# Kernel tuning notes

Hardware: AMD Instinct MI355X
Metric: run time of the kernel (lower is better)

## Reference

```python
import jax, jax.numpy as jnp
import numpy as np

S, H, T = 65536, 768, 6   # seq_len, hidden, n_types
K, WIN = 3, 15            # top-k starts, end-pointer window
TYPE_THRESH, START_THRESH = 0.3, 0.15


def setup_inputs() -> dict:
    key = jax.random.key(0)
    ks = jax.random.split(key, 9)
    sc = 0.02
    return {
        "token_embeds": jax.random.normal(ks[0], (S, H), dtype=jnp.float32),
        "W_start": jax.random.normal(ks[1], (H, T), dtype=jnp.float32) * sc,
        "b_start": jnp.zeros((T,), dtype=jnp.float32),
        "W_end": jax.random.normal(ks[2], (H, T), dtype=jnp.float32) * sc,
        "b_end": jnp.zeros((T,), dtype=jnp.float32),
        "W1": jax.random.normal(ks[3], (H, 64), dtype=jnp.float32) * sc,
        "b1": jnp.zeros((64,), dtype=jnp.float32),
        "W2": jax.random.normal(ks[4], (64, T), dtype=jnp.float32) * sc,
        "b2": jnp.zeros((T,), dtype=jnp.float32),
    }


def reference(token_embeds, W_start, b_start, W_end, b_end, W1, b1, W2, b2):
    # Pointer projections: (S, T)
    start_scores = token_embeds @ W_start + b_start
    end_scores = token_embeds @ W_end + b_end

    # Type confidence head on mean-pooled embedding (torch nn.GELU = exact erf)
    pooled = token_embeds.mean(axis=0)                      # (H,)
    h = jax.nn.gelu(pooled @ W1 + b1, approximate=False)    # (64,)
    type_conf = jax.nn.sigmoid(h @ W2 + b2)                 # (T,)

    # Softmax over sequence dim per type, then top-3 candidate starts per type
    s_probs = jax.nn.softmax(start_scores, axis=0)          # (S, T)
    top_vals, top_idx = jax.lax.top_k(s_probs.T, K)         # (T, K)

    # Windowed argmax over end_scores[s : s+15, t]
    pos = top_idx[:, :, None] + jnp.arange(WIN)
    in_range = pos < S
    pos_c = jnp.clip(pos, 0, S - 1)
    end_T = end_scores.T                                    # (T, S)
    window_vals = end_T[jnp.arange(T)[:, None, None], pos_c]
    window_vals = jnp.where(in_range, window_vals, -jnp.inf)
    e_off = jnp.argmax(window_vals, axis=-1)                # (T, K)

    starts = top_idx                                        # (T, K) int
    ends = top_idx + e_off + 1                              # exclusive end, matches e+1
    valid = (type_conf[:, None] >= TYPE_THRESH) & (top_vals >= START_THRESH)
    conf = jnp.where(valid, top_vals * type_conf[:, None], 0.0)  # (T, K)

    return conf, starts, ends, valid
```

## Files before the change

kernel.cpp:

```cpp
#include <hip/hip_runtime.h>
#include <math.h>

#define S_TOK 65536
#define H_DIM 768
#define T_TYPES 6
#define K_TOP 3
#define WIN 15
#define NBLK1 512
#define NWAVES (NBLK1 * 4)
#define ROWS_PER_WAVE (S_TOK / NWAVES)
#define POOL_CHUNKS 8
#define BLK_PER_CHUNK (NBLK1 / POOL_CHUNKS)

__device__ __forceinline__ void top3_insert(float v, int i,
    float& v0, float& v1, float& v2, int& i0, int& i1, int& i2)
{
    if (v > v0 || (v == v0 && i < i0)) {
        v2 = v1; i2 = i1; v1 = v0; i1 = i0; v0 = v; i0 = i;
    } else if (v > v1 || (v == v1 && i < i1)) {
        v2 = v1; i2 = i1; v1 = v; i1 = i;
    } else if (v > v2 || (v == v2 && i < i2)) {
        v2 = v; i2 = i;
    }
}

__device__ __forceinline__ void merge_state(
    float& M, float& se, float& v0, float& v1, float& v2,
    int& i0, int& i1, int& i2,
    float Mb, float seb, float w0, float w1, float w2,
    int j0, int j1, int j2)
{
    const float Mn = fmaxf(M, Mb);
    se = se * expf(M - Mn) + seb * expf(Mb - Mn);
    M = Mn;
    top3_insert(w0, j0, v0, v1, v2, i0, i1, i2);
    top3_insert(w1, j1, v0, v1, v2, i0, i1, i2);
    top3_insert(w2, j2, v0, v1, v2, i0, i1, i2);
}

__global__ __launch_bounds__(256, 2) void k_scores(
    const float* __restrict__ emb,
    const float* __restrict__ Wstart, const float* __restrict__ bstart,
    const float* __restrict__ Wend,   const float* __restrict__ bend,
    float* __restrict__ endS,
    float* __restrict__ partials,
    float* __restrict__ pooledPart)
{
    const int lane = threadIdx.x & 63;
    const int wib  = threadIdx.x >> 6;
    const int wave = blockIdx.x * 4 + wib;

    float wS[3][4][T_TYPES], wE[3][4][T_TYPES];
#pragma unroll
    for (int j = 0; j < 3; ++j)
#pragma unroll
        for (int c = 0; c < 4; ++c) {
            const int h = 4 * (lane + 64 * j) + c;
#pragma unroll
            for (int t = 0; t < T_TYPES; ++t) {
                wS[j][c][t] = Wstart[h * T_TYPES + t];
                wE[j][c][t] = Wend  [h * T_TYPES + t];
            }
        }

    float myBias = 0.0f;
    if (lane < T_TYPES)            myBias = bstart[lane];
    else if (lane < 2 * T_TYPES)   myBias = bend[lane - T_TYPES];

    float pool[3][4] = {};

    float M  = -3.402823466e38f, se = 0.0f;
    float v0 = -3.402823466e38f, v1 = v0, v2 = v0;
    int   i0 = -1, i1 = -1, i2 = -1;

    const int r0 = wave * ROWS_PER_WAVE;
    const float4* rowp = (const float4*)emb + (size_t)r0 * (H_DIM / 4);
    float4 c0 = rowp[lane], c1 = rowp[lane + 64], c2 = rowp[lane + 128];

    for (int r = r0; r < r0 + ROWS_PER_WAVE; ++r) {
        const float4* nextp = rowp + ((r + 1 < S_TOK) ? (H_DIM / 4) : 0);
        float4 n0 = nextp[lane], n1 = nextp[lane + 64], n2 = nextp[lane + 128];

        float acc[12];
#pragma unroll
        for (int a = 0; a < 12; ++a) acc[a] = 0.0f;

        const float4 ee[3] = {c0, c1, c2};
#pragma unroll
        for (int j = 0; j < 3; ++j) {
            const float ev[4] = {ee[j].x, ee[j].y, ee[j].z, ee[j].w};
#pragma unroll
            for (int c = 0; c < 4; ++c) {
                const float v = ev[c];
                pool[j][c] += v;
#pragma unroll
                for (int t = 0; t < T_TYPES; ++t) {
                    acc[t]           = fmaf(v, wS[j][c][t], acc[t]);
                    acc[T_TYPES + t] = fmaf(v, wE[j][c][t], acc[T_TYPES + t]);
                }
            }
        }

#pragma unroll
        for (int a = 0; a < 12; ++a) {
#pragma unroll
            for (int m = 1; m < 64; m <<= 1)
                acc[a] += __shfl_xor(acc[a], m, 64);
        }

        float v = acc[0];
#pragma unroll
        for (int a = 1; a < 12; ++a) v = (lane == a) ? acc[a] : v;
        v += myBias;

        if (lane < T_TYPES) {
            if (v > M) {
                se = se * expf(M - v) + 1.0f;
                v2 = v1; i2 = i1; v1 = v0; i1 = i0; v0 = v; i0 = r;
                M = v;
            } else {
                se += expf(v - M);
                if (v > v2 || (v == v2 && r < i2)) {
                    if (v > v1 || (v == v1 && r < i1)) {
                        v2 = v1; i2 = i1; v1 = v; i1 = r;
                    } else { v2 = v; i2 = r; }
                }
            }
        } else if (lane < 2 * T_TYPES) {
            endS[(size_t)(lane - T_TYPES) * S_TOK + r] = v;
        }

        c0 = n0; c1 = n1; c2 = n2; rowp = nextp;
    }

    if (lane < T_TYPES) {
        float* p = partials + ((size_t)wave * T_TYPES + lane) * 8;
        p[0] = M;  p[1] = se; p[2] = v0; p[3] = v1; p[4] = v2;
        p[5] = __int_as_float(i0);
        p[6] = __int_as_float(i1);
        p[7] = __int_as_float(i2);
    }

    __shared__ float lds[4][H_DIM];
#pragma unroll
    for (int j = 0; j < 3; ++j) {
        float4 pv = make_float4(pool[j][0], pool[j][1], pool[j][2], pool[j][3]);
        ((float4*)lds[wib])[lane + 64 * j] = pv;
    }
    __syncthreads();
    for (int h = threadIdx.x; h < H_DIM; h += 256) {
        pooledPart[(size_t)blockIdx.x * H_DIM + h] =
            (lds[0][h] + lds[1][h]) + (lds[2][h] + lds[3][h]);
    }
}

__global__ __launch_bounds__(1024) void k_mid(
    const float* __restrict__ partials,
    const float* __restrict__ pooledPart,
    float* __restrict__ pooled2,
    float* __restrict__ res)
{
    const int b = blockIdx.x;
    const int tid = threadIdx.x;

    if (b >= T_TYPES) {
        const int c = b - T_TYPES;
        if (tid < H_DIM) {
            const float* base = pooledPart + (size_t)c * BLK_PER_CHUNK * H_DIM + tid;
            float s0 = 0, s1 = 0, s2 = 0, s3 = 0;
            for (int i = 0; i < BLK_PER_CHUNK; i += 4) {
                s0 += base[(size_t)(i + 0) * H_DIM];
                s1 += base[(size_t)(i + 1) * H_DIM];
                s2 += base[(size_t)(i + 2) * H_DIM];
                s3 += base[(size_t)(i + 3) * H_DIM];
            }
            pooled2[c * H_DIM + tid] = (s0 + s1) + (s2 + s3);
        }
        return;
    }

    float M, se, v0, v1, v2; int i0, i1, i2;
    {
        const float* p = partials + ((size_t)tid * T_TYPES + b) * 8;
        M = p[0]; se = p[1]; v0 = p[2]; v1 = p[3]; v2 = p[4];
        i0 = __float_as_int(p[5]); i1 = __float_as_int(p[6]); i2 = __float_as_int(p[7]);
    }
    {
        const float* p = partials + ((size_t)(tid + 1024) * T_TYPES + b) * 8;
        merge_state(M, se, v0, v1, v2, i0, i1, i2,
                    p[0], p[1], p[2], p[3], p[4],
                    __float_as_int(p[5]), __float_as_int(p[6]), __float_as_int(p[7]));
    }

#pragma unroll
    for (int msk = 1; msk < 64; msk <<= 1) {
        const float Mb  = __shfl_xor(M,  msk, 64);
        const float seb = __shfl_xor(se, msk, 64);
        const float w0  = __shfl_xor(v0, msk, 64);
        const float w1  = __shfl_xor(v1, msk, 64);
        const float w2  = __shfl_xor(v2, msk, 64);
        const int   j0  = __shfl_xor(i0, msk, 64);
        const int   j1  = __shfl_xor(i1, msk, 64);
        const int   j2  = __shfl_xor(i2, msk, 64);
        merge_state(M, se, v0, v1, v2, i0, i1, i2, Mb, seb, w0, w1, w2, j0, j1, j2);
    }

    __shared__ float sm[16][8];
    if ((tid & 63) == 0) {
        const int w = tid >> 6;
        sm[w][0] = M;  sm[w][1] = se;
        sm[w][2] = v0; sm[w][3] = v1; sm[w][4] = v2;
        sm[w][5] = __int_as_float(i0);
        sm[w][6] = __int_as_float(i1);
        sm[w][7] = __int_as_float(i2);
    }
    __syncthreads();
    if (tid == 0) {
        for (int w = 1; w < 16; ++w) {
            merge_state(M, se, v0, v1, v2, i0, i1, i2,
                        sm[w][0], sm[w][1], sm[w][2], sm[w][3], sm[w][4],
                        __float_as_int(sm[w][5]), __float_as_int(sm[w][6]),
                        __float_as_int(sm[w][7]));
        }
        float* r = res + b * 8;
        r[0] = v0; r[1] = v1; r[2] = v2;
        r[3] = __int_as_float(i0);
        r[4] = __int_as_float(i1);
        r[5] = __int_as_float(i2);
        r[6] = M; r[7] = se;
    }
}

__global__ __launch_bounds__(256) void k_final(
    const float* __restrict__ pooled2,
    const float* __restrict__ W1, const float* __restrict__ b1,
    const float* __restrict__ W2, const float* __restrict__ b2,
    const float* __restrict__ endS, const float* __restrict__ res,
    float* __restrict__ out)
{
    const int tid = threadIdx.x;
    __shared__ float pl[H_DIM];
    for (int h = tid; h < H_DIM; h += 256) {
        float s = 0.0f;
#pragma unroll
        for (int c = 0; c < POOL_CHUNKS; ++c) s += pooled2[c * H_DIM + h];
        pl[h] = s * (1.0f / (float)S_TOK);
    }
    __syncthreads();

    __shared__ float hpart[4][64];
    {
        const int o = tid & 63, part = tid >> 6;
        const float* w = W1 + o;
        float z = 0.0f;
        for (int h = part * 192; h < part * 192 + 192; ++h)
            z = fmaf(pl[h], w[(size_t)h * 64], z);
        hpart[part][o] = z;
    }
    __syncthreads();

    __shared__ float hdn[64];
    if (tid < 64) {
        const float z = b1[tid] +
            ((hpart[0][tid] + hpart[1][tid]) + (hpart[2][tid] + hpart[3][tid]));
        hdn[tid] = 0.5f * z * (1.0f + erff(z * 0.7071067811865475f));
    }
    __syncthreads();

    __shared__ float tconf[T_TYPES];
    if (tid < T_TYPES) {
        float z = b2[tid];
        for (int i = 0; i < 64; ++i) z = fmaf(hdn[i], W2[i * T_TYPES + tid], z);
        tconf[tid] = 1.0f / (1.0f + expf(-z));
    }
    __syncthreads();

    if (tid < T_TYPES * K_TOP) {
        const int t = tid / K_TOP;
        const int k = tid % K_TOP;
        const float* r = res + t * 8;
        const float vraw = r[k];
        const int   idx  = __float_as_int(r[3 + k]);
        const float M    = r[6];
        const float SE   = r[7];
        const float prob = expf(vraw - M) / SE;

        const float* ecol = endS + (size_t)t * S_TOK;
        float best = -3.402823466e38f;
        int   boff = 0;
#pragma unroll
        for (int w = 0; w < WIN; ++w) {
            const int pos = idx + w;
            if (pos < S_TOK) {
                const float ev = ecol[pos];
                if (ev > best) { best = ev; boff = w; }
            }
        }
        const float tc = tconf[t];
        const bool valid = (tc >= 0.3f) && (prob >= 0.15f);
        out[tid]      = valid ? prob * tc : 0.0f;
        out[18 + tid] = (float)idx;
        out[36 + tid] = (float)(idx + boff + 1);
        out[54 + tid] = valid ? 1.0f : 0.0f;
    }
}

extern "C" void kernel_launch(void* const* d_in, const int* in_sizes, int n_in,
                              void* d_out, int out_size, void* d_ws, size_t ws_size,
                              hipStream_t stream)
{
    const float* emb    = (const float*)d_in[0];
    const float* Wstart = (const float*)d_in[1];
    const float* bstart = (const float*)d_in[2];
    const float* Wend   = (const float*)d_in[3];
    const float* bend   = (const float*)d_in[4];
    const float* W1     = (const float*)d_in[5];
    const float* b1     = (const float*)d_in[6];
    const float* W2     = (const float*)d_in[7];
    const float* b2     = (const float*)d_in[8];
    float* out = (float*)d_out;

    float* ws       = (float*)d_ws;
    float* endS     = ws;
    float* partials = endS + (size_t)T_TYPES * S_TOK;
    float* pp       = partials + (size_t)NWAVES * T_TYPES * 8;
    float* pooled2  = pp + (size_t)NBLK1 * H_DIM;
    float* res      = pooled2 + (size_t)POOL_CHUNKS * H_DIM;

    k_scores<<<NBLK1, 256, 0, stream>>>(emb, Wstart, bstart, Wend, bend,
                                        endS, partials, pp);
    k_mid<<<T_TYPES + POOL_CHUNKS, 1024, 0, stream>>>(partials, pp, pooled2, res);
    k_final<<<1, 256, 0, stream>>>(pooled2, W1, b1, W2, b2, endS, res, out);
}
```

Baseline: 349.2 us.

## Use transpose-style butterfly reduction for 12 dot products and move W1 GEMV into k_mid

Replaces the 12 independent full 64-lane xor-shuffle reductions per row with a recursive-halving butterfly, where each stage exchanges half the remaining accumulators so the 12 sums end up on designated lanes. This cuts the shuffle count per row sharply, since cross-lane reduction dominated the per-row work. Lane-to-output mapping changes accordingly. Separately, the pooled-embedding W1 projection is split across the 8 pooling-chunk blocks in k_mid, so the single-block k_final does less serial work.

New measurement: 341.0 us. -2.3%, faster.

```diff
diff --git a/kernel.cpp b/kernel.cpp
--- a/kernel.cpp
+++ b/kernel.cpp
@@ -50,6 +50,15 @@
     const int wib  = threadIdx.x >> 6;
     const int wave = blockIdx.x * 4 + wib;
 
+    const bool b5 = (lane & 32) != 0;
+    const bool b4 = (lane & 16) != 0;
+    const bool b3 = (lane & 8)  != 0;
+    const bool b2 = (lane & 4)  != 0;
+    const int  sem = (b5 ? 6 : 0) + (b4 ? 3 : 0) + (b3 ? 2 : (b2 ? 1 : 0));
+    const bool desig   = ((lane & 3) == 0) && !(b3 && b2);
+    const bool isStart = desig && !b5;
+    const bool isEnd   = desig && b5;
+
     float wS[3][4][T_TYPES], wE[3][4][T_TYPES];
 #pragma unroll
     for (int j = 0; j < 3; ++j)
@@ -64,8 +73,8 @@
         }
 
     float myBias = 0.0f;
-    if (lane < T_TYPES)            myBias = bstart[lane];
-    else if (lane < 2 * T_TYPES)   myBias = bend[lane - T_TYPES];
+    if (isStart) myBias = bstart[sem];
+    if (isEnd)   myBias = bend[sem - T_TYPES];
 
     float pool[3][4] = {};
 
@@ -101,19 +110,40 @@
             }
         }
 
-#pragma unroll
-        for (int a = 0; a < 12; ++a) {
-#pragma unroll
-            for (int m = 1; m < 64; m <<= 1)
-                acc[a] += __shfl_xor(acc[a], m, 64);
-        }
-
-        float v = acc[0];
-#pragma unroll
-        for (int a = 1; a < 12; ++a) v = (lane == a) ? acc[a] : v;
-        v += myBias;
-
-        if (lane < T_TYPES) {
+        float na[6];
+#pragma unroll
+        for (int t = 0; t < 6; ++t) {
+            const float snd  = b5 ? acc[t] : acc[t + 6];
+            const float keep = b5 ? acc[t + 6] : acc[t];
+            na[t] = keep + __shfl_xor(snd, 32, 64);
+        }
+        float nb[3];
+#pragma unroll
+        for (int t = 0; t < 3; ++t) {
+            const float snd  = b4 ? na[t] : na[t + 3];
+            const float keep = b4 ? na[t + 3] : na[t];
+            nb[t] = keep + __shfl_xor(snd, 16, 64);
+        }
+        float nc0, nc1;
+        {
+            const float snd  = b3 ? nb[2] : nb[0];
+            const float keep = b3 ? nb[2] : nb[0];
+            nc0 = keep + __shfl_xor(b3 ? nb[0] : nb[2], 8, 64);
+            (void)snd;
+            nc1 = nb[1] + __shfl_xor(nb[1], 8, 64);
+        }
+        float d;
+        {
+            const float snd  = (b3 || b2) ? nc0 : nc1;
+            const float keep = (!b3 && b2) ? nc1 : nc0;
+            d = keep + __shfl_xor(snd, 4, 64);
+        }
+        d += __shfl_xor(d, 2, 64);
+        d += __shfl_xor(d, 1, 64);
+
+        const float v = d + myBias;
+
+        if (isStart) {
             if (v > M) {
                 se = se * expf(M - v) + 1.0f;
                 v2 = v1; i2 = i1; v1 = v0; i1 = i0; v0 = v; i0 = r;
@@ -126,15 +156,15 @@
                     } else { v2 = v; i2 = r; }
                 }
             }
-        } else if (lane < 2 * T_TYPES) {
-            endS[(size_t)(lane - T_TYPES) * S_TOK + r] = v;
+        } else if (isEnd) {
+            endS[(size_t)(sem - T_TYPES) * S_TOK + r] = v;
         }
 
         c0 = n0; c1 = n1; c2 = n2; rowp = nextp;
     }
 
-    if (lane < T_TYPES) {
-        float* p = partials + ((size_t)wave * T_TYPES + lane) * 8;
+    if (isStart) {
+        float* p = partials + ((size_t)wave * T_TYPES + sem) * 8;
         p[0] = M;  p[1] = se; p[2] = v0; p[3] = v1; p[4] = v2;
         p[5] = __int_as_float(i0);
         p[6] = __int_as_float(i1);
@@ -157,7 +187,8 @@
 __global__ __launch_bounds__(1024) void k_mid(
     const float* __restrict__ partials,
     const float* __restrict__ pooledPart,
-    float* __restrict__ pooled2,
+    const float* __restrict__ W1,
+    float* __restrict__ zpart,
     float* __restrict__ res)
 {
     const int b = blockIdx.x;
@@ -165,6 +196,7 @@
 
     if (b >= T_TYPES) {
         const int c = b - T_TYPES;
+        __shared__ float pl[H_DIM];
         if (tid < H_DIM) {
             const float* base = pooledPart + (size_t)c * BLK_PER_CHUNK * H_DIM + tid;
             float s0 = 0, s1 = 0, s2 = 0, s3 = 0;
@@ -174,7 +206,22 @@
                 s2 += base[(size_t)(i + 2) * H_DIM];
                 s3 += base[(size_t)(i + 3) * H_DIM];
             }
-            pooled2[c * H_DIM + tid] = (s0 + s1) + (s2 + s3);
+            pl[tid] = (s0 + s1) + (s2 + s3);
+        }
+        __syncthreads();
+        const int o = tid & 63, seg = tid >> 6;
+        float z = 0.0f;
+        const int h0 = seg * 48;
+        for (int i = 0; i < 48; ++i)
+            z = fmaf(pl[h0 + i], W1[(size_t)(h0 + i) * 64 + o], z);
+        __shared__ float zred[16][64];
+        zred[seg][o] = z;
+        __syncthreads();
+        if (tid < 64) {
+            float s = 0.0f;
+#pragma unroll
+            for (int g = 0; g < 16; ++g) s += zred[g][tid];
+            zpart[c * 64 + tid] = s;
         }
         return;
     }
@@ -232,37 +279,19 @@
 }
 
 __global__ __launch_bounds__(256) void k_final(
-    const float* __restrict__ pooled2,
-    const float* __restrict__ W1, const float* __restrict__ b1,
+    const float* __restrict__ zpart,
+    const float* __restrict__ b1,
     const float* __restrict__ W2, const float* __restrict__ b2,
     const float* __restrict__ endS, const float* __restrict__ res,
     float* __restrict__ out)
 {
     const int tid = threadIdx.x;
-    __shared__ float pl[H_DIM];
-    for (int h = tid; h < H_DIM; h += 256) {
-        float s = 0.0f;
-#pragma unroll
-        for (int c = 0; c < POOL_CHUNKS; ++c) s += pooled2[c * H_DIM + h];
-        pl[h] = s * (1.0f / (float)S_TOK);
-    }
-    __syncthreads();
-
-    __shared__ float hpart[4][64];
-    {
-        const int o = tid & 63, part = tid >> 6;
-        const float* w = W1 + o;
-        float z = 0.0f;
-        for (int h = part * 192; h < part * 192 + 192; ++h)
-            z = fmaf(pl[h], w[(size_t)h * 64], z);
-        hpart[part][o] = z;
-    }
-    __syncthreads();
-
     __shared__ float hdn[64];
     if (tid < 64) {
-        const float z = b1[tid] +
-            ((hpart[0][tid] + hpart[1][tid]) + (hpart[2][tid] + hpart[3][tid]));
+        float zs = 0.0f;
+#pragma unroll
+        for (int c = 0; c < POOL_CHUNKS; ++c) zs += zpart[c * 64 + tid];
+        const float z = zs * (1.0f / (float)S_TOK) + b1[tid];
         hdn[tid] = 0.5f * z * (1.0f + erff(z * 0.7071067811865475f));
     }
     __syncthreads();
@@ -324,11 +353,11 @@
     float* endS     = ws;
     float* partials = endS + (size_t)T_TYPES * S_TOK;
     float* pp       = partials + (size_t)NWAVES * T_TYPES * 8;
-    float* pooled2  = pp + (size_t)NBLK1 * H_DIM;
-    float* res      = pooled2 + (size_t)POOL_CHUNKS * H_DIM;
+    float* zpart    = pp + (size_t)NBLK1 * H_DIM;
+    float* res      = zpart + (size_t)POOL_CHUNKS * 64;
 
     k_scores<<<NBLK1, 256, 0, stream>>>(emb, Wstart, bstart, Wend, bend,
                                         endS, partials, pp);
-    k_mid<<<T_TYPES + POOL_CHUNKS, 1024, 0, stream>>>(partials, pp, pooled2, res);
-    k_final<<<1, 256, 0, stream>>>(pooled2, W1, b1, W2, b2, endS, res, out);
-}
+    k_mid<<<T_TYPES + POOL_CHUNKS, 1024, 0, stream>>>(partials, pp, W1, zpart, res);
+    k_final<<<1, 256, 0, stream>>>(zpart, b1, W2, b2, endS, res, out);
+}
```
